# Kernel optimization log

Measured on AMD Instinct MI355X. Metric: run time of the kernel, lower is better.

Reference implementation:

```python
import jax, jax.numpy as jnp
import numpy as np

B, L, DIM, DQK = 4, 8192, 512, 512
THRESH = 0.5
TARGET_N = 6.0
RATIO_W = 0.03
LR_DIFF = 0.75
EPS = 1e-8


def setup_inputs() -> dict:
    key = jax.random.key(0)
    k1, k2, k3 = jax.random.split(key, 3)
    tokens = jax.random.normal(k1, (B, L, DIM), dtype=jnp.float32)
    # Linear(dim, 2*dqk, bias=False) weight, torch layout [out, in]
    Wqk = jax.random.normal(k2, (2 * DQK, DIM), dtype=jnp.float32) / np.sqrt(DIM).astype(np.float32)
    start_key = jax.random.normal(k3, (DQK,), dtype=jnp.float32) * 0.01  # heads=1
    return {"tokens": tokens, "Wqk": Wqk, "start_key": start_key}


def _straight_through(t, value):
    return t + jax.lax.stop_gradient(value - t)


def _frac_gradient(t, frac):
    # forward = t, backward grad scaled by frac
    return _straight_through(t * frac, t)


def _cosine_sim(a, b):
    dot = jnp.sum(a * b, axis=-1)
    na = jnp.maximum(jnp.sqrt(jnp.sum(a * a, axis=-1)), EPS)
    nb = jnp.maximum(jnp.sqrt(jnp.sum(b * b, axis=-1)), EPS)
    return dot / (na * nb)


def _assoc_scan(gates, x):
    # h_t = gates_t * h_{t-1} + x_t along axis 1 (inclusive first-order scan)
    def comb(l, r):
        al, bl = l
        ar, br = r
        return al * ar, br + ar * bl
    _, h = jax.lax.associative_scan(comb, (gates[..., None], x), axis=1)
    return h


def reference(tokens, Wqk, start_key):
    Bn, Ln, D = tokens.shape
    qk = jnp.einsum('bnd,ed->bne', tokens, Wqk)          # [B, L, 2*DQK]
    queries, keys = qk[..., :DQK], qk[..., DQK:]
    # key for position i is key_{i-1}, with learned start key at position 0
    keys_shift = jnp.concatenate(
        [jnp.broadcast_to(start_key, (Bn, 1, DQK)), keys[:, :-1]], axis=1)
    cos = _cosine_sim(queries, keys_shift)               # [B, L]
    probs = (1.0 - cos) * 0.5
    boundary = (probs > THRESH).at[:, 0].set(True)       # [B, L] bool
    num_chunks = boundary.sum(axis=-1)                   # [B]

    # stable compaction: boundary positions first, in order
    order = jnp.argsort(jnp.logical_not(boundary).astype(jnp.int32), axis=1)  # [B, L]
    ar = jnp.arange(Ln)
    chunk_mask = ar[None, :] < num_chunks[:, None]       # valid chunk slots
    pos = jnp.where(chunk_mask, order, Ln)               # boundary positions, sentinel L
    next_pos = jnp.concatenate([pos[:, 1:], jnp.full((Bn, 1), Ln, dtype=pos.dtype)], axis=1)
    chunk_lens = jnp.where(chunk_mask, next_pos - pos, 0)  # [B, L] int

    gathered = jnp.take_along_axis(tokens, order[..., None], axis=1)  # [B, L, D]
    boundary_probs = jnp.where(chunk_mask, jnp.take_along_axis(probs, order, axis=1), 0.0)
    gates = 1.0 - boundary_probs                         # padded slots -> 1 (matches torch, never read)
    downsampled = gathered * boundary_probs[..., None]   # padded slots -> 0

    confidence = jnp.where(boundary, probs, 1.0 - probs)
    scale = _straight_through(confidence, 1.0)           # forward value 1.0

    # aux ratio loss (with straight-through soft boundary fraction)
    Nt = TARGET_N
    F_hard = boundary.astype(probs.dtype)
    F_soft = jax.nn.sigmoid(probs - THRESH)
    F = _straight_through(F_soft, F_hard)
    Gm = probs.mean(axis=-1)
    Fm = F.mean(axis=-1)
    aux = (Nt / (Nt - 1.0)) * ((Nt - 1.0) * Fm * Gm + (1.0 - Fm) * (1.0 - Gm))
    weighted_aux_loss = aux.mean() * RATIO_W

    downsampled_out = _frac_gradient(downsampled, 1.0 / LR_DIFF)

    # ---- upsample path (the returned closure in the torch module) ----
    scanned = _assoc_scan(gates, downsampled_out)        # smooth across chunks
    rank = jnp.cumsum(boundary.astype(jnp.int32), axis=1) - 1  # chunk id of each token
    upsampled = jnp.take_along_axis(scanned, rank[..., None], axis=1)  # [B, L, D]
    upsampled = upsampled * scale[..., None]
    upsampled = _frac_gradient(upsampled, LR_DIFF)

    return downsampled_out, upsampled, weighted_aux_loss
```

## Files before the change

### kernel.cpp

```cpp
#include <hip/hip_runtime.h>
#include <cstdint>
#include <cstddef>

#define L 8192
#define BATCH 4
#define DQK 512
#define M_TOT (BATCH*L)
#define EPSC 1e-8f

typedef __attribute__((ext_vector_type(8))) short bf16x8;
typedef __attribute__((ext_vector_type(4))) float f32x4;
typedef __attribute__((ext_vector_type(8))) unsigned short u16x8;

__device__ __forceinline__ unsigned short bf16_rne(float x) {
  union { float f; unsigned u; } v; v.f = x;
  unsigned r = v.u + 0x7fffu + ((v.u >> 16) & 1u);
  return (unsigned short)(r >> 16);
}
__device__ __forceinline__ float bf16_tof(unsigned short b) {
  union { unsigned u; float f; } v; v.u = ((unsigned)b) << 16;
  return v.f;
}
__device__ __forceinline__ void gload_lds16(const void* g, void* l) {
  __builtin_amdgcn_global_load_lds(
      (const __attribute__((address_space(1))) unsigned int*)g,
      (__attribute__((address_space(3))) unsigned int*)l, 16, 0, 0);
}

__global__ __launch_bounds__(256) void k_split(const float* __restrict__ tokens,
                                               const float* __restrict__ Wqk,
                                               unsigned short* __restrict__ A1,
                                               unsigned short* __restrict__ A2,
                                               unsigned short* __restrict__ A3,
                                               unsigned short* __restrict__ W1,
                                               unsigned short* __restrict__ W2,
                                               unsigned short* __restrict__ W3) {
  const float* src; unsigned short *d1, *d2, *d3; size_t e0;
  if (blockIdx.x < 8192) {
    src = tokens; d1 = A1; d2 = A2; d3 = A3;
    e0 = ((size_t)blockIdx.x * 256 + threadIdx.x) * 8;
  } else {
    src = Wqk; d1 = W1; d2 = W2; d3 = W3;
    e0 = ((size_t)(blockIdx.x - 8192) * 256 + threadIdx.x) * 8;
  }
  float v[8];
  *(float4*)&v[0] = *(const float4*)(src + e0);
  *(float4*)&v[4] = *(const float4*)(src + e0 + 4);
  unsigned short o1[8], o2[8], o3[8];
  #pragma unroll
  for (int j = 0; j < 8; ++j) {
    float x = v[j];
    unsigned short b1 = bf16_rne(x);
    float r1 = x - bf16_tof(b1);
    unsigned short b2 = bf16_rne(r1);
    float r2 = r1 - bf16_tof(b2);
    unsigned short b3 = bf16_rne(r2);
    o1[j] = b1; o2[j] = b2; o3[j] = b3;
  }
  *(u16x8*)(d1 + e0) = *(u16x8*)o1;
  *(u16x8*)(d2 + e0) = *(u16x8*)o2;
  *(u16x8*)(d3 + e0) = *(u16x8*)o3;
}

__global__ __launch_bounds__(256, 3) void k_gemm_bf16(
    const unsigned short* __restrict__ A1, const unsigned short* __restrict__ A2,
    const unsigned short* __restrict__ A3,
    const unsigned short* __restrict__ W1, const unsigned short* __restrict__ W2,
    const unsigned short* __restrict__ W3,
    float* __restrict__ C) {
  __shared__ unsigned short lds[6 * 512 * 8];
  const int g = (blockIdx.x & 7) * 256 + (blockIdx.x >> 3);
  const int bx = g & 7;
  const int by = g >> 3;
  const int t = threadIdx.x;
  const int lane = t & 63;
  const int w = t >> 6;
  const int wr = w >> 1, wc = w & 1;

  f32x4 acc[4][4];
  #pragma unroll
  for (int i = 0; i < 4; ++i)
    #pragma unroll
    for (int j = 0; j < 4; ++j) acc[i][j] = (f32x4){0.f, 0.f, 0.f, 0.f};

  const unsigned short* srcA[3] = {A1, A2, A3};
  const unsigned short* srcW[3] = {W1, W2, W3};
  const int arow = by * 128;
  const int wrow = bx * 128;
  const int kg = lane >> 4;
  const int fr = lane & 15;

  for (int ks = 0; ks < 16; ++ks) {
    __syncthreads();
    const int kofs = ks * 32;
    #pragma unroll
    for (int s = 0; s < 3; ++s) {
      #pragma unroll
      for (int it = 0; it < 2; ++it) {
        const int p = it * 256 + t;
        const int row = p & 127, pg = p >> 7;
        gload_lds16(srcA[s] + (size_t)(arow + row) * 512 + kofs + pg * 8,
                    &lds[(s * 512 + p) * 8]);
        gload_lds16(srcW[s] + (size_t)(wrow + row) * 512 + kofs + pg * 8,
                    &lds[((3 + s) * 512 + p) * 8]);
      }
    }
    __syncthreads();

    bf16x8 bfr[4][3];
    #pragma unroll
    for (int nf = 0; nf < 4; ++nf) {
      const int row = wc * 64 + nf * 16 + fr;
      #pragma unroll
      for (int s = 0; s < 3; ++s)
        bfr[nf][s] = *(const bf16x8*)&lds[(((3 + s) * 512) + kg * 128 + row) * 8];
    }
    #pragma unroll
    for (int mf = 0; mf < 4; ++mf) {
      const int row = wr * 64 + mf * 16 + fr;
      bf16x8 a1 = *(const bf16x8*)&lds[((0 * 512) + kg * 128 + row) * 8];
      bf16x8 a2 = *(const bf16x8*)&lds[((1 * 512) + kg * 128 + row) * 8];
      bf16x8 a3 = *(const bf16x8*)&lds[((2 * 512) + kg * 128 + row) * 8];
      #pragma unroll
      for (int nf = 0; nf < 4; ++nf) {
        f32x4 c = acc[mf][nf];
        c = __builtin_amdgcn_mfma_f32_16x16x32_bf16(a1, bfr[nf][0], c, 0, 0, 0);
        c = __builtin_amdgcn_mfma_f32_16x16x32_bf16(a1, bfr[nf][1], c, 0, 0, 0);
        c = __builtin_amdgcn_mfma_f32_16x16x32_bf16(a2, bfr[nf][0], c, 0, 0, 0);
        c = __builtin_amdgcn_mfma_f32_16x16x32_bf16(a2, bfr[nf][1], c, 0, 0, 0);
        c = __builtin_amdgcn_mfma_f32_16x16x32_bf16(a1, bfr[nf][2], c, 0, 0, 0);
        c = __builtin_amdgcn_mfma_f32_16x16x32_bf16(a3, bfr[nf][0], c, 0, 0, 0);
        acc[mf][nf] = c;
      }
    }
  }
  const int fq = lane >> 4;
  #pragma unroll
  for (int mf = 0; mf < 4; ++mf) {
    #pragma unroll
    for (int nf = 0; nf < 4; ++nf) {
      const int col = bx * 128 + wc * 64 + nf * 16 + fr;
      #pragma unroll
      for (int r = 0; r < 4; ++r) {
        const int rrow = by * 128 + wr * 64 + mf * 16 + fq * 4 + r;
        C[(size_t)rrow * 1024 + col] = acc[mf][nf][r];
      }
    }
  }
}

__global__ __launch_bounds__(256) void k_gemm(const float* __restrict__ A,
                                              const float* __restrict__ W,
                                              float* __restrict__ C) {
  __shared__ float As[8][128];
  __shared__ float Bs[8][128];
  const int bx = blockIdx.x & 7;
  const int by = blockIdx.x >> 3;
  const int t  = threadIdx.x;
  const int tx = t & 15, ty = t >> 4;
  const int lr = t >> 1;
  const int lc = (t & 1) * 4;
  const float* Ag = A + (size_t)(by*128 + lr)*512 + lc;
  const float* Wg = W + (size_t)(bx*128 + lr)*512 + lc;
  float acc[8][8];
  #pragma unroll
  for (int i=0;i<8;i++)
    #pragma unroll
    for (int j=0;j<8;j++) acc[i][j]=0.f;

  for (int k0 = 0; k0 < 512; k0 += 8) {
    float4 av = *(const float4*)(Ag + k0);
    float4 bv = *(const float4*)(Wg + k0);
    __syncthreads();
    As[lc+0][lr]=av.x; As[lc+1][lr]=av.y; As[lc+2][lr]=av.z; As[lc+3][lr]=av.w;
    Bs[lc+0][lr]=bv.x; Bs[lc+1][lr]=bv.y; Bs[lc+2][lr]=bv.z; Bs[lc+3][lr]=bv.w;
    __syncthreads();
    #pragma unroll
    for (int kk=0;kk<8;kk++) {
      float af[8], bf[8];
      *(float4*)&af[0] = *(const float4*)&As[kk][ty*8];
      *(float4*)&af[4] = *(const float4*)&As[kk][ty*8+4];
      *(float4*)&bf[0] = *(const float4*)&Bs[kk][tx*8];
      *(float4*)&bf[4] = *(const float4*)&Bs[kk][tx*8+4];
      #pragma unroll
      for (int i=0;i<8;i++)
        #pragma unroll
        for (int j=0;j<8;j++)
          acc[i][j] = fmaf(af[i], bf[j], acc[i][j]);
    }
  }
  const int crow = by*128 + ty*8;
  const int ccol = bx*128 + tx*8;
  #pragma unroll
  for (int i=0;i<8;i++) {
    float* cp = C + (size_t)(crow+i)*1024 + ccol;
    *(float4*)cp     = make_float4(acc[i][0],acc[i][1],acc[i][2],acc[i][3]);
    *(float4*)(cp+4) = make_float4(acc[i][4],acc[i][5],acc[i][6],acc[i][7]);
  }
}

__global__ __launch_bounds__(256) void k_cos(const float* __restrict__ qk,
                                             const float* __restrict__ start_key,
                                             float* __restrict__ probs) {
  const int wid = threadIdx.x >> 6;
  const int lane = threadIdx.x & 63;
  const int p = blockIdx.x*4 + wid;
  const int n = p & (L-1);
  const float* q  = qk + (size_t)p*1024;
  const float* ks = (n==0) ? start_key : (qk + (size_t)(p-1)*1024 + 512);
  float dot=0.f, nq=0.f, nk=0.f;
  const int e0 = lane*8;
  #pragma unroll
  for (int j=0;j<8;j+=4) {
    float4 qv = *(const float4*)(q+e0+j);
    float4 kv = *(const float4*)(ks+e0+j);
    dot = fmaf(qv.x,kv.x,dot); dot = fmaf(qv.y,kv.y,dot);
    dot = fmaf(qv.z,kv.z,dot); dot = fmaf(qv.w,kv.w,dot);
    nq  = fmaf(qv.x,qv.x,nq);  nq  = fmaf(qv.y,qv.y,nq);
    nq  = fmaf(qv.z,qv.z,nq);  nq  = fmaf(qv.w,qv.w,nq);
    nk  = fmaf(kv.x,kv.x,nk);  nk  = fmaf(kv.y,kv.y,nk);
    nk  = fmaf(kv.z,kv.z,nk);  nk  = fmaf(kv.w,kv.w,nk);
  }
  #pragma unroll
  for (int m=32;m>=1;m>>=1) {
    dot += __shfl_xor(dot,m);
    nq  += __shfl_xor(nq,m);
    nk  += __shfl_xor(nk,m);
  }
  if (lane==0) {
    float na = fmaxf(sqrtf(nq), EPSC);
    float nb = fmaxf(sqrtf(nk), EPSC);
    float c  = dot/(na*nb);
    probs[p] = 0.5f*(1.f - c);
  }
}

__global__ __launch_bounds__(1024) void k_scan_bd(const float* __restrict__ probs,
                                                  int* __restrict__ bpos,
                                                  int* __restrict__ num_chunks,
                                                  float* __restrict__ auxvals) {
  const int b = blockIdx.x;
  const float* pb = probs + b*L;
  const int t = threadIdx.x;
  float pv[8]; int bd[8];
  const int base = t*8;
  float psum=0.f; int cnt=0;
  #pragma unroll
  for (int j=0;j<8;j++) {
    pv[j] = pb[base+j];
    bd[j] = (base+j == 0) || (pv[j] > 0.5f);
    cnt += bd[j];
    psum += pv[j];
  }
  const int lane = t & 63, w = t >> 6;
  int x = cnt;
  #pragma unroll
  for (int off=1; off<64; off<<=1) {
    int y = __shfl_up(x, off);
    if (lane >= off) x += y;
  }
  float ps = psum;
  #pragma unroll
  for (int m=32;m>=1;m>>=1) ps += __shfl_xor(ps, m);
  __shared__ int wsum[16]; __shared__ int wpre[17]; __shared__ float fsum[16];
  if (lane == 63) wsum[w] = x;
  if (lane == 0)  fsum[w] = ps;
  __syncthreads();
  if (t == 0) {
    int run = 0; float tot = 0.f;
    for (int i=0;i<16;i++) { wpre[i] = run; run += wsum[i]; tot += fsum[i]; }
    wpre[16] = run;
    num_chunks[b] = run;
    float Gm = tot / (float)L;
    float Fm = (float)run / (float)L;
    auxvals[b] = 1.2f * (5.f*Fm*Gm + (1.f-Fm)*(1.f-Gm));
  }
  __syncthreads();
  int rank = wpre[w] + (x - cnt);
  #pragma unroll
  for (int j=0;j<8;j++) {
    if (bd[j]) { bpos[b*L + rank] = base + j; rank++; }
  }
}

__global__ __launch_bounds__(512) void k_scan_local(const float* __restrict__ tokens,
                                                    const float* __restrict__ probs,
                                                    const int* __restrict__ bpos,
                                                    const int* __restrict__ num_chunks,
                                                    float* __restrict__ local_h,
                                                    float* __restrict__ gpref,
                                                    float* __restrict__ hend,
                                                    float* __restrict__ Pseg,
                                                    float* __restrict__ down) {
  const int b = blockIdx.x >> 6;
  const int s = blockIdx.x & 63;
  const int c = threadIdx.x;
  const int nc = num_chunks[b];
  const int i0 = s*128;
  const int seg = b*64 + s;
  const int z0 = (i0 > nc) ? i0 : nc;
  for (int i = z0; i < i0 + 128; ++i)
    down[((size_t)(b*L + i))*512 + c] = 0.f;
  if (i0 >= nc) {
    hend[(size_t)seg*512 + c] = 0.f;
    if (c==0) Pseg[seg] = 1.f;
    return;
  }
  const int iend = (i0+128 < nc) ? i0+128 : nc;
  const int cntc = iend - i0;
  __shared__ float p_s[128];
  __shared__ int n_s[128];
  if (c < cntc) {
    int n = bpos[b*L + i0 + c];
    n_s[c] = n;
    p_s[c] = probs[b*L + n];
  }
  __syncthreads();
  float h = 0.f, gp = 1.f;
  for (int i = i0; i < iend; ++i) {
    const int ii = i - i0;
    const float p = p_s[ii];
    const float g = 1.f - p;
    const float x = tokens[((size_t)(b*L + n_s[ii]))*512 + c] * p;
    h = fmaf(g, h, x);
    gp *= g;
    down[((size_t)(b*L + i))*512 + c] = x;
    local_h[((size_t)(b*L + i))*512 + c] = h;
    if (c==0) gpref[b*L + i] = gp;
  }
  hend[(size_t)seg*512 + c] = h;
  if (c==0) Pseg[seg] = gp;
}

__global__ __launch_bounds__(512) void k_seg_combine(const float* __restrict__ hend,
                                                     const float* __restrict__ Pseg,
                                                     float* __restrict__ carry_in) {
  const int b = blockIdx.x;
  const int c = threadIdx.x;
  float carry = 0.f;
  for (int s = 0; s < 64; ++s) {
    const int seg = b*64 + s;
    carry_in[(size_t)seg*512 + c] = carry;
    carry = fmaf(Pseg[seg], carry, hend[(size_t)seg*512 + c]);
  }
}

__global__ __launch_bounds__(512) void k_expand(const float* __restrict__ local_h,
                                                const float* __restrict__ gpref,
                                                const float* __restrict__ carry_in,
                                                const int* __restrict__ bpos,
                                                const int* __restrict__ num_chunks,
                                                float* __restrict__ up) {
  const int b = blockIdx.x >> 6;
  const int s = blockIdx.x & 63;
  const int c = threadIdx.x;
  const int nc = num_chunks[b];
  const int i0 = s*128;
  if (i0 >= nc) return;
  const int iend = (i0+128 < nc) ? i0+128 : nc;
  const int cntc = iend - i0;
  __shared__ int n_s[129];
  __shared__ float gp_s[128];
  if (c < cntc) { n_s[c] = bpos[b*L + i0 + c]; gp_s[c] = gpref[b*L + i0 + c]; }
  if (c == 0)   n_s[cntc] = (iend < nc) ? bpos[b*L + iend] : L;
  __syncthreads();
  const float carry = carry_in[((size_t)(b*64 + s))*512 + c];
  for (int i = i0; i < iend; ++i) {
    const int ii = i - i0;
    const float hf = fmaf(gp_s[ii], carry, local_h[((size_t)(b*L + i))*512 + c]);
    const int n0 = n_s[ii], n1 = n_s[ii+1];
    for (int n = n0; n < n1; ++n)
      up[((size_t)(b*L + n))*512 + c] = hf;
  }
}

__global__ void k_final(const float* __restrict__ auxvals, float* __restrict__ outp) {
  outp[0] = (auxvals[0]+auxvals[1]+auxvals[2]+auxvals[3]) * 0.25f * 0.03f;
}

extern "C" void kernel_launch(void* const* d_in, const int* in_sizes, int n_in,
                              void* d_out, int out_size, void* d_ws, size_t ws_size,
                              hipStream_t stream) {
  const float* tokens    = (const float*)d_in[0];
  const float* Wqk       = (const float*)d_in[1];
  const float* start_key = (const float*)d_in[2];
  float* out  = (float*)d_out;
  float* down = out;
  float* up   = out + (size_t)M_TOT*512;
  float* qk   = out;

  char* ws = (char*)d_ws;
  const size_t A_BYTES = (size_t)M_TOT*512*2;
  const size_t W_BYTES = (size_t)1024*512*2;
  const size_t STAGED_BASE = 3*A_BYTES + 3*W_BYTES;
  const size_t SMALL_BYTES = (size_t)M_TOT*4*3 + (size_t)BATCH*64*512*4*2
                           + (size_t)BATCH*64*4 + BATCH*4*2 + 256;
  const bool staged = ws_size >= STAGED_BASE + SMALL_BYTES;

  unsigned short* A1 = (unsigned short*)ws;
  unsigned short* A2 = (unsigned short*)(ws + A_BYTES);
  unsigned short* A3 = (unsigned short*)(ws + 2*A_BYTES);
  unsigned short* W1 = (unsigned short*)(ws + 3*A_BYTES);
  unsigned short* W2 = (unsigned short*)(ws + 3*A_BYTES + W_BYTES);
  unsigned short* W3 = (unsigned short*)(ws + 3*A_BYTES + 2*W_BYTES);

  float* local_h = (float*)ws;
  size_t off = staged ? STAGED_BASE : (size_t)M_TOT*512*4;
  float* probs    = (float*)(ws + off); off += (size_t)M_TOT*4;
  int*   bpos     = (int*)  (ws + off); off += (size_t)M_TOT*4;
  float* gpref    = (float*)(ws + off); off += (size_t)M_TOT*4;
  float* hend     = (float*)(ws + off); off += (size_t)BATCH*64*512*4;
  float* carry_in = (float*)(ws + off); off += (size_t)BATCH*64*512*4;
  float* Pseg     = (float*)(ws + off); off += (size_t)BATCH*64*4;
  int*   num_chunks = (int*)(ws + off); off += (size_t)BATCH*4;
  float* auxvals  = (float*)(ws + off); off += (size_t)BATCH*4;

  if (staged) {
    k_split<<<8448, 256, 0, stream>>>(tokens, Wqk, A1, A2, A3, W1, W2, W3);
    k_gemm_bf16<<<2048, 256, 0, stream>>>(A1, A2, A3, W1, W2, W3, qk);
  } else {
    k_gemm<<<2048, 256, 0, stream>>>(tokens, Wqk, qk);
  }
  k_cos<<<M_TOT/4, 256, 0, stream>>>(qk, start_key, probs);
  k_scan_bd<<<BATCH, 1024, 0, stream>>>(probs, bpos, num_chunks, auxvals);
  k_scan_local<<<BATCH*64, 512, 0, stream>>>(tokens, probs, bpos, num_chunks,
                                             local_h, gpref, hend, Pseg, down);
  k_seg_combine<<<BATCH, 512, 0, stream>>>(hend, Pseg, carry_in);
  k_expand<<<BATCH*64, 512, 0, stream>>>(local_h, gpref, carry_in, bpos, num_chunks, up);
  k_final<<<1, 1, 0, stream>>>(auxvals, out + (size_t)2*M_TOT*512);
}
```

Measured before the change: 411.4 us.

## Recompute local scan in expand, parallelize segment combine, use 32x32 MFMA

The local scan no longer writes per-chunk hidden states and gate prefixes to workspace. The expand kernel instead rereads the gathered tokens and probs and redoes the recurrence starting from the carry-in, which removes a full-size intermediate write and read. The serial per-batch segment combine becomes a parallel Hillis-Steele scan over 64 segments across 256 blocks. The bf16 GEMM also switches from 16x16x32 to 32x32x16 MFMA tiles. Together these drop large intermediate traffic at the cost of a second gather of tokens and some recomputation.

Result: no change. 419.6 us (+2.0%).

```diff
diff --git a/kernel.cpp b/kernel.cpp
--- a/kernel.cpp
+++ b/kernel.cpp
@@ -10,6 +10,7 @@
 
 typedef __attribute__((ext_vector_type(8))) short bf16x8;
 typedef __attribute__((ext_vector_type(4))) float f32x4;
+typedef __attribute__((ext_vector_type(16))) float f32x16;
 typedef __attribute__((ext_vector_type(8))) unsigned short u16x8;
 
 __device__ __forceinline__ unsigned short bf16_rne(float x) {
@@ -77,18 +78,20 @@
   const int w = t >> 6;
   const int wr = w >> 1, wc = w & 1;
 
-  f32x4 acc[4][4];
-  #pragma unroll
-  for (int i = 0; i < 4; ++i)
-    #pragma unroll
-    for (int j = 0; j < 4; ++j) acc[i][j] = (f32x4){0.f, 0.f, 0.f, 0.f};
+  f32x16 acc[2][2];
+  #pragma unroll
+  for (int i = 0; i < 2; ++i)
+    #pragma unroll
+    for (int j = 0; j < 2; ++j)
+      #pragma unroll
+      for (int r = 0; r < 16; ++r) acc[i][j][r] = 0.f;
 
   const unsigned short* srcA[3] = {A1, A2, A3};
   const unsigned short* srcW[3] = {W1, W2, W3};
   const int arow = by * 128;
   const int wrow = bx * 128;
-  const int kg = lane >> 4;
-  const int fr = lane & 15;
+  const int l31 = lane & 31;
+  const int loct = lane >> 5;
 
   for (int ks = 0; ks < 16; ++ks) {
     __syncthreads();
@@ -107,42 +110,50 @@
     }
     __syncthreads();
 
-    bf16x8 bfr[4][3];
-    #pragma unroll
-    for (int nf = 0; nf < 4; ++nf) {
-      const int row = wc * 64 + nf * 16 + fr;
-      #pragma unroll
-      for (int s = 0; s < 3; ++s)
-        bfr[nf][s] = *(const bf16x8*)&lds[(((3 + s) * 512) + kg * 128 + row) * 8];
-    }
-    #pragma unroll
-    for (int mf = 0; mf < 4; ++mf) {
-      const int row = wr * 64 + mf * 16 + fr;
-      bf16x8 a1 = *(const bf16x8*)&lds[((0 * 512) + kg * 128 + row) * 8];
-      bf16x8 a2 = *(const bf16x8*)&lds[((1 * 512) + kg * 128 + row) * 8];
-      bf16x8 a3 = *(const bf16x8*)&lds[((2 * 512) + kg * 128 + row) * 8];
-      #pragma unroll
-      for (int nf = 0; nf < 4; ++nf) {
-        f32x4 c = acc[mf][nf];
-        c = __builtin_amdgcn_mfma_f32_16x16x32_bf16(a1, bfr[nf][0], c, 0, 0, 0);
-        c = __builtin_amdgcn_mfma_f32_16x16x32_bf16(a1, bfr[nf][1], c, 0, 0, 0);
-        c = __builtin_amdgcn_mfma_f32_16x16x32_bf16(a2, bfr[nf][0], c, 0, 0, 0);
-        c = __builtin_amdgcn_mfma_f32_16x16x32_bf16(a2, bfr[nf][1], c, 0, 0, 0);
-        c = __builtin_amdgcn_mfma_f32_16x16x32_bf16(a1, bfr[nf][2], c, 0, 0, 0);
-        c = __builtin_amdgcn_mfma_f32_16x16x32_bf16(a3, bfr[nf][0], c, 0, 0, 0);
-        acc[mf][nf] = c;
+    bf16x8 bfr[2][2][3];
+    #pragma unroll
+    for (int nf = 0; nf < 2; ++nf) {
+      const int row = wc * 64 + nf * 32 + l31;
+      #pragma unroll
+      for (int kk = 0; kk < 2; ++kk) {
+        const int oct = kk * 2 + loct;
+        #pragma unroll
+        for (int s = 0; s < 3; ++s)
+          bfr[nf][kk][s] = *(const bf16x8*)&lds[(((3 + s) * 512) + oct * 128 + row) * 8];
       }
     }
-  }
-  const int fq = lane >> 4;
-  #pragma unroll
-  for (int mf = 0; mf < 4; ++mf) {
-    #pragma unroll
-    for (int nf = 0; nf < 4; ++nf) {
-      const int col = bx * 128 + wc * 64 + nf * 16 + fr;
-      #pragma unroll
-      for (int r = 0; r < 4; ++r) {
-        const int rrow = by * 128 + wr * 64 + mf * 16 + fq * 4 + r;
+    #pragma unroll
+    for (int mf = 0; mf < 2; ++mf) {
+      const int row = wr * 64 + mf * 32 + l31;
+      #pragma unroll
+      for (int kk = 0; kk < 2; ++kk) {
+        const int oct = kk * 2 + loct;
+        bf16x8 a1 = *(const bf16x8*)&lds[((0 * 512) + oct * 128 + row) * 8];
+        bf16x8 a2 = *(const bf16x8*)&lds[((1 * 512) + oct * 128 + row) * 8];
+        bf16x8 a3 = *(const bf16x8*)&lds[((2 * 512) + oct * 128 + row) * 8];
+        #pragma unroll
+        for (int nf = 0; nf < 2; ++nf) {
+          f32x16 c = acc[mf][nf];
+          c = __builtin_amdgcn_mfma_f32_32x32x16_bf16(a1, bfr[nf][kk][0], c, 0, 0, 0);
+          c = __builtin_amdgcn_mfma_f32_32x32x16_bf16(a1, bfr[nf][kk][1], c, 0, 0, 0);
+          c = __builtin_amdgcn_mfma_f32_32x32x16_bf16(a2, bfr[nf][kk][0], c, 0, 0, 0);
+          c = __builtin_amdgcn_mfma_f32_32x32x16_bf16(a2, bfr[nf][kk][1], c, 0, 0, 0);
+          c = __builtin_amdgcn_mfma_f32_32x32x16_bf16(a1, bfr[nf][kk][2], c, 0, 0, 0);
+          c = __builtin_amdgcn_mfma_f32_32x32x16_bf16(a3, bfr[nf][kk][0], c, 0, 0, 0);
+          acc[mf][nf] = c;
+        }
+      }
+    }
+  }
+  const int ro = 4 * loct;
+  #pragma unroll
+  for (int mf = 0; mf < 2; ++mf) {
+    #pragma unroll
+    for (int nf = 0; nf < 2; ++nf) {
+      const int col = bx * 128 + wc * 64 + nf * 32 + l31;
+      #pragma unroll
+      for (int r = 0; r < 16; ++r) {
+        const int rrow = by * 128 + wr * 64 + mf * 32 + ro + (r & 3) + 8 * (r >> 2);
         C[(size_t)rrow * 1024 + col] = acc[mf][nf][r];
       }
     }
@@ -287,8 +298,6 @@
                                                     const float* __restrict__ probs,
                                                     const int* __restrict__ bpos,
                                                     const int* __restrict__ num_chunks,
-                                                    float* __restrict__ local_h,
-                                                    float* __restrict__ gpref,
                                                     float* __restrict__ hend,
                                                     float* __restrict__ Pseg,
                                                     float* __restrict__ down) {
@@ -325,31 +334,44 @@
     h = fmaf(g, h, x);
     gp *= g;
     down[((size_t)(b*L + i))*512 + c] = x;
-    local_h[((size_t)(b*L + i))*512 + c] = h;
-    if (c==0) gpref[b*L + i] = gp;
   }
   hend[(size_t)seg*512 + c] = h;
   if (c==0) Pseg[seg] = gp;
 }
 
-__global__ __launch_bounds__(512) void k_seg_combine(const float* __restrict__ hend,
-                                                     const float* __restrict__ Pseg,
-                                                     float* __restrict__ carry_in) {
-  const int b = blockIdx.x;
-  const int c = threadIdx.x;
-  float carry = 0.f;
-  for (int s = 0; s < 64; ++s) {
-    const int seg = b*64 + s;
-    carry_in[(size_t)seg*512 + c] = carry;
-    carry = fmaf(Pseg[seg], carry, hend[(size_t)seg*512 + c]);
-  }
-}
-
-__global__ __launch_bounds__(512) void k_expand(const float* __restrict__ local_h,
-                                                const float* __restrict__ gpref,
-                                                const float* __restrict__ carry_in,
+__global__ __launch_bounds__(512) void k_seg_scan(const float* __restrict__ hend,
+                                                  const float* __restrict__ Pseg,
+                                                  float* __restrict__ carry_in) {
+  const int b  = blockIdx.x >> 6;
+  const int gch = blockIdx.x & 63;
+  const int sg = threadIdx.x & 63;
+  const int cl = threadIdx.x >> 6;
+  const int ch = gch*8 + cl;
+  const int seg = b*64 + sg;
+  float h = hend[(size_t)seg*512 + ch];
+  float P = Pseg[seg];
+  __shared__ float sh[512], sP[512];
+  const int idx = cl*64 + sg;
+  #pragma unroll
+  for (int off=1; off<64; off<<=1) {
+    sh[idx] = h; sP[idx] = P;
+    __syncthreads();
+    if (sg >= off) {
+      h = fmaf(P, sh[idx-off], h);
+      P = P * sP[idx-off];
+    }
+    __syncthreads();
+  }
+  sh[idx] = h;
+  __syncthreads();
+  carry_in[(size_t)seg*512 + ch] = (sg==0) ? 0.f : sh[idx-1];
+}
+
+__global__ __launch_bounds__(512) void k_expand(const float* __restrict__ tokens,
+                                                const float* __restrict__ probs,
                                                 const int* __restrict__ bpos,
                                                 const int* __restrict__ num_chunks,
+                                                const float* __restrict__ carry_in,
                                                 float* __restrict__ up) {
   const int b = blockIdx.x >> 6;
   const int s = blockIdx.x & 63;
@@ -359,18 +381,25 @@
   if (i0 >= nc) return;
   const int iend = (i0+128 < nc) ? i0+128 : nc;
   const int cntc = iend - i0;
+  __shared__ float p_s[128];
   __shared__ int n_s[129];
-  __shared__ float gp_s[128];
-  if (c < cntc) { n_s[c] = bpos[b*L + i0 + c]; gp_s[c] = gpref[b*L + i0 + c]; }
+  if (c < cntc) {
+    int n = bpos[b*L + i0 + c];
+    n_s[c] = n;
+    p_s[c] = probs[b*L + n];
+  }
   if (c == 0)   n_s[cntc] = (iend < nc) ? bpos[b*L + iend] : L;
   __syncthreads();
-  const float carry = carry_in[((size_t)(b*64 + s))*512 + c];
+  float h = carry_in[((size_t)(b*64 + s))*512 + c];
   for (int i = i0; i < iend; ++i) {
     const int ii = i - i0;
-    const float hf = fmaf(gp_s[ii], carry, local_h[((size_t)(b*L + i))*512 + c]);
+    const float p = p_s[ii];
+    const float g = 1.f - p;
+    const float x = tokens[((size_t)(b*L + n_s[ii]))*512 + c] * p;
+    h = fmaf(g, h, x);
     const int n0 = n_s[ii], n1 = n_s[ii+1];
     for (int n = n0; n < n1; ++n)
-      up[((size_t)(b*L + n))*512 + c] = hf;
+      up[((size_t)(b*L + n))*512 + c] = h;
   }
 }
 
@@ -393,7 +422,7 @@
   const size_t A_BYTES = (size_t)M_TOT*512*2;
   const size_t W_BYTES = (size_t)1024*512*2;
   const size_t STAGED_BASE = 3*A_BYTES + 3*W_BYTES;
-  const size_t SMALL_BYTES = (size_t)M_TOT*4*3 + (size_t)BATCH*64*512*4*2
+  const size_t SMALL_BYTES = (size_t)M_TOT*4*2 + (size_t)BATCH*64*512*4*2
                            + (size_t)BATCH*64*4 + BATCH*4*2 + 256;
   const bool staged = ws_size >= STAGED_BASE + SMALL_BYTES;
 
@@ -404,11 +433,9 @@
   unsigned short* W2 = (unsigned short*)(ws + 3*A_BYTES + W_BYTES);
   unsigned short* W3 = (unsigned short*)(ws + 3*A_BYTES + 2*W_BYTES);
 
-  float* local_h = (float*)ws;
-  size_t off = staged ? STAGED_BASE : (size_t)M_TOT*512*4;
+  size_t off = staged ? STAGED_BASE : 0;
   float* probs    = (float*)(ws + off); off += (size_t)M_TOT*4;
   int*   bpos     = (int*)  (ws + off); off += (size_t)M_TOT*4;
-  float* gpref    = (float*)(ws + off); off += (size_t)M_TOT*4;
   float* hend     = (float*)(ws + off); off += (size_t)BATCH*64*512*4;
   float* carry_in = (float*)(ws + off); off += (size_t)BATCH*64*512*4;
   float* Pseg     = (float*)(ws + off); off += (size_t)BATCH*64*4;
@@ -424,8 +451,8 @@
   k_cos<<<M_TOT/4, 256, 0, stream>>>(qk, start_key, probs);
   k_scan_bd<<<BATCH, 1024, 0, stream>>>(probs, bpos, num_chunks, auxvals);
   k_scan_local<<<BATCH*64, 512, 0, stream>>>(tokens, probs, bpos, num_chunks,
-                                             local_h, gpref, hend, Pseg, down);
-  k_seg_combine<<<BATCH, 512, 0, stream>>>(hend, Pseg, carry_in);
-  k_expand<<<BATCH*64, 512, 0, stream>>>(local_h, gpref, carry_in, bpos, num_chunks, up);
+                                             hend, Pseg, down);
+  k_seg_scan<<<BATCH*64, 512, 0, stream>>>(hend, Pseg, carry_in);
+  k_expand<<<BATCH*64, 512, 0, stream>>>(tokens, probs, bpos, num_chunks, carry_in, up);
   k_final<<<1, 1, 0, stream>>>(auxvals, out + (size_t)2*M_TOT*512);
 }
```
